# Kernel optimization log

Hardware: AMD Instinct MI355X
Metric: run time of the kernel (lower is better)

## Reference

```python
import jax, jax.numpy as jnp
import numpy as np

N_QUBITS = 4


def _apply_1q(state, U, q):
    """Apply a 2x2 gate U (shape (2,2) or batched (b,2,2)) to qubit q of state (b,2,2,2,2)."""
    s = jnp.moveaxis(state, 1 + q, -1)
    if U.ndim == 3:
        s = jnp.einsum('bij,b...j->b...i', U, s)
    else:
        s = jnp.einsum('ij,b...j->b...i', U, s)
    return jnp.moveaxis(s, -1, 1 + q)


def _apply_cnot(state, c, t):
    """CNOT with control qubit c, target qubit t."""
    s = jnp.moveaxis(state, (1 + c, 1 + t), (-2, -1))
    s = jnp.stack([s[..., 0, :], s[..., 1, ::-1]], axis=-2)  # flip target where control=1
    return jnp.moveaxis(s, (-2, -1), (1 + c, 1 + t))


def _ry_mat(theta):
    """Batched RY matrix, theta (b,) -> (b,2,2) complex64."""
    c = jnp.cos(theta * 0.5).astype(jnp.complex64)
    s = jnp.sin(theta * 0.5).astype(jnp.complex64)
    return jnp.stack([jnp.stack([c, -s], -1), jnp.stack([s, c], -1)], -2)


def _rot_mat(phi, theta, omega):
    """PennyLane Rot(phi, theta, omega) = RZ(omega) RY(theta) RZ(phi), scalar params -> (2,2) complex64."""
    c = jnp.cos(theta * 0.5).astype(jnp.complex64)
    s = jnp.sin(theta * 0.5).astype(jnp.complex64)
    ep = jnp.exp(-0.5j * (phi + omega).astype(jnp.complex64))  # e^{-i(phi+omega)/2}
    em = jnp.exp(0.5j * (phi - omega).astype(jnp.complex64))   # e^{+i(phi-omega)/2}
    row0 = jnp.stack([c * ep, -s * em])
    row1 = jnp.stack([s * jnp.conj(em), c * jnp.conj(ep)])
    return jnp.stack([row0, row1])


def _circuit(x, params):
    b = x.shape[0]
    n_layers = params.shape[0]
    # The 64 sequential RY(x[i]) on wire i%4 commute (same axis) and compose
    # additively: RY(a)RY(b) = RY(a+b). Exact same math, fused.
    angles = x.reshape(b, -1, N_QUBITS).sum(axis=1)  # (b, 4)
    state = jnp.zeros((b,) + (2,) * N_QUBITS, jnp.complex64)
    state = state.at[(slice(None),) + (0,) * N_QUBITS].set(1.0)  # |0000>
    for q in range(N_QUBITS):
        state = _apply_1q(state, _ry_mat(angles[:, q]), q)
    for l in range(n_layers):
        for q in range(N_QUBITS):
            state = _apply_1q(state, _rot_mat(params[l, q, 0], params[l, q, 1], params[l, q, 2]), q)
        for q in range(N_QUBITS - 1):
            state = _apply_cnot(state, q, q + 1)
        state = _apply_cnot(state, N_QUBITS - 1, 0)
    probs = jnp.abs(state) ** 2  # (b,2,2,2,2), real
    z = jnp.array([1.0, -1.0], jnp.float32)
    evs = []
    for q in range(N_QUBITS):
        zq = z.reshape((1,) + (1,) * q + (2,) + (1,) * (N_QUBITS - 1 - q))
        evs.append((probs * zq).sum(axis=tuple(range(1, N_QUBITS + 1))))
    return jnp.stack(evs, axis=-1)  # (b, 4): <Z_0..Z_3>


def setup_inputs() -> dict:
    key = jax.random.key(0)
    k1, k2 = jax.random.split(key)
    x = jax.random.normal(k1, (131072, 64), dtype=jnp.float32)
    params = jax.random.normal(k2, (2, 4, 3), dtype=jnp.float32)
    return {"x": x, "params": params}


def reference(x, params):
    return _circuit(x, params)
```

## Files before the change

kernel.cpp:

```cpp
#include <hip/hip_runtime.h>
#include <hip/hip_bf16.h>


__global__ void qc_setup(const float* __restrict__ params, float* __restrict__ M)
{
    __shared__ float Ur[16][16];
    __shared__ float Ui[16][16];
    const int tid = threadIdx.x;

    if (tid < 16) {
        const int col = tid;
        float ur[16], ui[16];
        #pragma unroll
        for (int k = 0; k < 16; ++k) { ur[k] = (k == col) ? 1.f : 0.f; ui[k] = 0.f; }

        #pragma unroll
        for (int l = 0; l < 2; ++l) {
            #pragma unroll
            for (int q = 0; q < 4; ++q) {
                const float phi = params[l*12 + q*3 + 0];
                const float th  = params[l*12 + q*3 + 1];
                const float om  = params[l*12 + q*3 + 2];
                const float ct = cosf(0.5f*th), st = sinf(0.5f*th);
                const float ap = 0.5f*(phi + om), am = 0.5f*(phi - om);
                const float cap = cosf(ap), sap = sinf(ap);
                const float cam = cosf(am), sam = sinf(am);
                const float u00r =  ct*cap, u00i = -ct*sap;
                const float u01r = -st*cam, u01i = -st*sam;
                const float u10r =  st*cam, u10i = -st*sam;
                const float u11r =  ct*cap, u11i =  ct*sap;
                const int bit = 1 << (3 - q);
                #pragma unroll
                for (int k = 0; k < 16; ++k) {
                    if (k & bit) continue;
                    const int k1 = k | bit;
                    const float arr = ur[k],  aii = ui[k];
                    const float brr = ur[k1], bii = ui[k1];
                    ur[k]  = u00r*arr - u00i*aii + u01r*brr - u01i*bii;
                    ui[k]  = u00r*aii + u00i*arr + u01r*bii + u01i*brr;
                    ur[k1] = u10r*arr - u10i*aii + u11r*brr - u11i*bii;
                    ui[k1] = u10r*aii + u10i*arr + u11r*bii + u11i*brr;
                }
            }
            const int cs[4] = {0,1,2,3}, ts[4] = {1,2,3,0};
            #pragma unroll
            for (int e = 0; e < 4; ++e) {
                const int cb = 3 - cs[e], tb = 3 - ts[e];
                float nr[16], ni[16];
                #pragma unroll
                for (int k = 0; k < 16; ++k) {
                    const int src = ((k >> cb) & 1) ? (k ^ (1 << tb)) : k;
                    nr[k] = ur[src]; ni[k] = ui[src];
                }
                #pragma unroll
                for (int k = 0; k < 16; ++k) { ur[k] = nr[k]; ui[k] = ni[k]; }
            }
        }
        #pragma unroll
        for (int k = 0; k < 16; ++k) { Ur[k][col] = ur[k]; Ui[k][col] = ui[k]; }
    }
    __syncthreads();

    const int i = tid >> 4, j = tid & 15;
    float m0 = 0.f, m1 = 0.f, m2 = 0.f, m3 = 0.f;
    #pragma unroll
    for (int k = 0; k < 16; ++k) {
        const float dot = Ur[k][i]*Ur[k][j] + Ui[k][i]*Ui[k][j];
        m0 += ((k >> 3) & 1) ? -dot : dot;
        m1 += ((k >> 2) & 1) ? -dot : dot;
        m2 += ((k >> 1) & 1) ? -dot : dot;
        m3 += ( k       & 1) ? -dot : dot;
    }
    const float sc = (i == j) ? 1.f : 2.f;
    float4 o; o.x = m0*sc; o.y = m1*sc; o.z = m2*sc; o.w = m3*sc;
    reinterpret_cast<float4*>(M)[i*16 + j] = o;
}

__global__ __launch_bounds__(256) void qc_main(const float4* __restrict__ x4,
                                               const float4* __restrict__ Mg,
                                               float4* __restrict__ out4)
{
    const int b = blockIdx.x * 256 + threadIdx.x;
    const float4* row = x4 + ((size_t)b << 4);

    float a0 = 0.f, a1 = 0.f, a2 = 0.f, a3 = 0.f;
    #pragma unroll
    for (int j = 0; j < 16; ++j) {
        const float4 v = row[j];
        a0 += v.x; a1 += v.y; a2 += v.z; a3 += v.w;
    }

    float c0,s0,c1,s1,c2,s2,c3,s3;
    __sincosf(0.5f*a0, &s0, &c0);
    __sincosf(0.5f*a1, &s1, &c1);
    __sincosf(0.5f*a2, &s2, &c2);
    __sincosf(0.5f*a3, &s3, &c3);

    float p23[4] = { c2*c3, c2*s3, s2*c3, s2*s3 };
    float p123[8];
    #pragma unroll
    for (int t = 0; t < 4; ++t) { p123[t] = c1*p23[t]; p123[4+t] = s1*p23[t]; }
    float psi[16];
    #pragma unroll
    for (int u = 0; u < 8; ++u) { psi[u] = c0*p123[u]; psi[8+u] = s0*p123[u]; }

    float ax = 0.f, ay = 0.f, az = 0.f, aw = 0.f;
    #pragma unroll
    for (int i = 0; i < 16; ++i) {
        #pragma unroll
        for (int j = i; j < 16; ++j) {
            const float pp = psi[i] * psi[j];
            const float4 m = Mg[i*16 + j];
            ax = fmaf(pp, m.x, ax);
            ay = fmaf(pp, m.y, ay);
            az = fmaf(pp, m.z, az);
            aw = fmaf(pp, m.w, aw);
        }
    }
    float4 r; r.x = ax; r.y = ay; r.z = az; r.w = aw;
    out4[b] = r;
}

extern "C" void kernel_launch(void* const* d_in, const int* in_sizes, int n_in,
                              void* d_out, int out_size, void* d_ws, size_t ws_size,
                              hipStream_t stream)
{
    const float* x      = (const float*)d_in[0];
    const float* params = (const float*)d_in[1];
    float*       out    = (float*)d_out;
    float*       M      = (float*)d_ws;

    qc_setup<<<1, 256, 0, stream>>>(params, M);

    const int batch = in_sizes[0] / 64;
    qc_main<<<batch / 256, 256, 0, stream>>>(
        (const float4*)x, (const float4*)M, (float4*)out);
}
```

Baseline: 84.16 us.

## Expand quadratic form in trig basis to reduce per-sample terms

Rewrites the per-sample quadratic form psi^T M psi, where psi is a product state of cos/sin half-angles, using double-angle identities. Each qubit factor becomes a combination of {1, cos a, sin a}, so the expectation is an 81-term tensor sum with coefficients precomputed once in the setup kernel. The main kernel drops the 136 pairwise products and loads, replacing them with 81 coefficient FMAs over four float4 lanes. The setup kernel gains an extra LDS stage and sync to build the coefficients. Since the main kernel is likely bound by reading x, the compute saving may not show up in the time.

```diff
diff --git a/kernel.cpp b/kernel.cpp
--- a/kernel.cpp
+++ b/kernel.cpp
@@ -2,10 +2,11 @@
 #include <hip/hip_bf16.h>
 
 
-__global__ void qc_setup(const float* __restrict__ params, float* __restrict__ M)
+__global__ void qc_setup(const float* __restrict__ params, float4* __restrict__ C4)
 {
-    __shared__ float Ur[16][16];
-    __shared__ float Ui[16][16];
+    __shared__ float  Ur[16][16];
+    __shared__ float  Ui[16][16];
+    __shared__ float4 Mlds[256];
     const int tid = threadIdx.x;
 
     if (tid < 16) {
@@ -61,23 +62,52 @@
     }
     __syncthreads();
 
-    const int i = tid >> 4, j = tid & 15;
-    float m0 = 0.f, m1 = 0.f, m2 = 0.f, m3 = 0.f;
-    #pragma unroll
-    for (int k = 0; k < 16; ++k) {
-        const float dot = Ur[k][i]*Ur[k][j] + Ui[k][i]*Ui[k][j];
-        m0 += ((k >> 3) & 1) ? -dot : dot;
-        m1 += ((k >> 2) & 1) ? -dot : dot;
-        m2 += ((k >> 1) & 1) ? -dot : dot;
-        m3 += ( k       & 1) ? -dot : dot;
+    {
+        const int i = tid >> 4, j = tid & 15;
+        float m0 = 0.f, m1 = 0.f, m2 = 0.f, m3 = 0.f;
+        #pragma unroll
+        for (int k = 0; k < 16; ++k) {
+            const float dot = Ur[k][i]*Ur[k][j] + Ui[k][i]*Ui[k][j];
+            m0 += ((k >> 3) & 1) ? -dot : dot;
+            m1 += ((k >> 2) & 1) ? -dot : dot;
+            m2 += ((k >> 1) & 1) ? -dot : dot;
+            m3 += ( k       & 1) ? -dot : dot;
+        }
+        float4 o; o.x = m0; o.y = m1; o.z = m2; o.w = m3;
+        Mlds[tid] = o;
     }
-    const float sc = (i == j) ? 1.f : 2.f;
-    float4 o; o.x = m0*sc; o.y = m1*sc; o.z = m2*sc; o.w = m3*sc;
-    reinterpret_cast<float4*>(M)[i*16 + j] = o;
+    __syncthreads();
+
+    if (tid < 81) {
+        int d[4]; int tt = tid;
+        d[0] = tt % 3; tt /= 3; d[1] = tt % 3; tt /= 3; d[2] = tt % 3; d[3] = tt / 3;
+        float ax = 0.f, ay = 0.f, az = 0.f, aw = 0.f;
+        #pragma unroll
+        for (int combo = 0; combo < 16; ++combo) {
+            int i = 0, j = 0; float w = 1.f;
+            #pragma unroll
+            for (int q = 0; q < 4; ++q) {
+                const int o = (combo >> q) & 1;
+                int bi, bj; float wq;
+                if (d[q] == 2)      { bi = o; bj = 1 - o; wq = 0.5f; }
+                else if (d[q] == 1) { bi = o; bj = o;     wq = o ? -0.5f : 0.5f; }
+                else                { bi = o; bj = o;     wq = 0.5f; }
+                i |= bi << (3 - q); j |= bj << (3 - q);
+                w *= wq;
+            }
+            const float4 m = Mlds[i*16 + j];
+            ax = fmaf(w, m.x, ax);
+            ay = fmaf(w, m.y, ay);
+            az = fmaf(w, m.z, az);
+            aw = fmaf(w, m.w, aw);
+        }
+        float4 c; c.x = ax; c.y = ay; c.z = az; c.w = aw;
+        C4[tid] = c;
+    }
 }
 
 __global__ __launch_bounds__(256) void qc_main(const float4* __restrict__ x4,
-                                               const float4* __restrict__ Mg,
+                                               const float4* __restrict__ C4,
                                                float4* __restrict__ out4)
 {
     const int b = blockIdx.x * 256 + threadIdx.x;
@@ -91,31 +121,33 @@
     }
 
     float c0,s0,c1,s1,c2,s2,c3,s3;
-    __sincosf(0.5f*a0, &s0, &c0);
-    __sincosf(0.5f*a1, &s1, &c1);
-    __sincosf(0.5f*a2, &s2, &c2);
-    __sincosf(0.5f*a3, &s3, &c3);
+    __sincosf(a0, &s0, &c0);
+    __sincosf(a1, &s1, &c1);
+    __sincosf(a2, &s2, &c2);
+    __sincosf(a3, &s3, &c3);
 
-    float p23[4] = { c2*c3, c2*s3, s2*c3, s2*s3 };
-    float p123[8];
+    const float g0[3] = {1.f, c0, s0};
+    const float g1[3] = {1.f, c1, s1};
+    const float g2[3] = {1.f, c2, s2};
+    const float g3[3] = {1.f, c3, s3};
+    float P01[9], P23[9];
     #pragma unroll
-    for (int t = 0; t < 4; ++t) { p123[t] = c1*p23[t]; p123[4+t] = s1*p23[t]; }
-    float psi[16];
-    #pragma unroll
-    for (int u = 0; u < 8; ++u) { psi[u] = c0*p123[u]; psi[8+u] = s0*p123[u]; }
+    for (int e1 = 0; e1 < 3; ++e1)
+        #pragma unroll
+        for (int e0 = 0; e0 < 3; ++e0) {
+            P01[e0 + 3*e1] = g0[e0] * g1[e1];
+            P23[e0 + 3*e1] = g2[e0] * g3[e1];
+        }
 
     float ax = 0.f, ay = 0.f, az = 0.f, aw = 0.f;
     #pragma unroll
-    for (int i = 0; i < 16; ++i) {
-        #pragma unroll
-        for (int j = i; j < 16; ++j) {
-            const float pp = psi[i] * psi[j];
-            const float4 m = Mg[i*16 + j];
-            ax = fmaf(pp, m.x, ax);
-            ay = fmaf(pp, m.y, ay);
-            az = fmaf(pp, m.z, az);
-            aw = fmaf(pp, m.w, aw);
-        }
+    for (int t = 0; t < 81; ++t) {
+        const float T = P01[t % 9] * P23[t / 9];
+        const float4 m = C4[t];
+        ax = fmaf(T, m.x, ax);
+        ay = fmaf(T, m.y, ay);
+        az = fmaf(T, m.z, az);
+        aw = fmaf(T, m.w, aw);
     }
     float4 r; r.x = ax; r.y = ay; r.z = az; r.w = aw;
     out4[b] = r;
@@ -128,11 +160,11 @@
     const float* x      = (const float*)d_in[0];
     const float* params = (const float*)d_in[1];
     float*       out    = (float*)d_out;
-    float*       M      = (float*)d_ws;
+    float4*      C4     = (float4*)d_ws;
 
-    qc_setup<<<1, 256, 0, stream>>>(params, M);
+    qc_setup<<<1, 256, 0, stream>>>(params, C4);
 
     const int batch = in_sizes[0] / 64;
     qc_main<<<batch / 256, 256, 0, stream>>>(
-        (const float4*)x, (const float4*)M, (float4*)out);
+        (const float4*)x, (const float4*)C4, (float4*)out);
 }
```

Result: no change. 84.84 us (+0.8%).
